# Kernel tuning notes

Measured on AMD Instinct MI355X. Metric: run time of the kernel, lower is better.

## Reference

```python
import jax, jax.numpy as jnp
import numpy as np

B, N = 8, 1000
EMB, K, F1E, F1V, MSG = 4, 3, 2, 3, 2


def cross_concat(h):
    # h: [b, n, d] -> [b, n, n, 2d], interleaving (h_i, h_j) per feature (stack axis=-1 then reshape)
    b, n, d = h.shape
    hi = jnp.broadcast_to(h[:, :, None, :], (b, n, n, d))
    hj = jnp.broadcast_to(h[:, None, :, :], (b, n, n, d))
    return jnp.stack((hi, hj), axis=-1).reshape(b, n, n, 2 * d)


def setup_inputs() -> dict:
    key = jax.random.key(0)
    ks = jax.random.split(key, 16)
    p = lambda k, s: (jax.random.normal(k, s, dtype=jnp.float32) * 0.1)
    return {
        "x": jax.random.normal(ks[0], (B, N), dtype=jnp.float32),
        "W1_emb": p(ks[1], (1, EMB)), "b1_emb": p(ks[2], (EMB,)),
        "W2_emb": p(ks[3], (1, EMB)), "b2_emb": p(ks[4], (EMB,)),
        "W_f1e": p(ks[5], (2 * EMB, F1E)), "b_f1e": p(ks[6], (F1E,)),
        "W_f2e": p(ks[7], (2 * F1V, K)), "b_f2e": p(ks[8], (K,)),
        "W_fk": p(ks[9], (K, 2 * EMB, MSG)), "b_fk": p(ks[10], (K, MSG)),
        "W_f1v": p(ks[11], (F1E, F1V)), "b_f1v": p(ks[12], (F1V,)),
        "W_f2v": p(ks[13], (MSG + 1, 1)), "b_f2v": p(ks[14], (1,)),
    }


def reference(x, W1_emb, b1_emb, W2_emb, b2_emb, W_f1e, b_f1e, W_f2e, b_f2e,
              W_fk, b_fk, W_f1v, b_f1v, W_f2v, b_f2v):
    x_ = x[..., None]                                  # [B,N,1]
    h1 = x_ @ W1_emb + b1_emb                          # [B,N,EMB]
    c = cross_concat(h1)                               # [B,N,N,2*EMB]
    h = jnp.sum(c @ W_f1e + b_f1e, axis=2)             # [B,N,F1E]
    h2 = h @ W_f1v + b_f1v                             # [B,N,F1V]
    c2 = cross_concat(h2)                              # [B,N,N,2*F1V]
    hsum = jnp.sum(c2, axis=0)                         # [N,N,2*F1V] (sum over batch)
    edge_logits = hsum @ W_f2e + b_f2e                 # [N,N,K]
    edge_probs = jax.nn.softmax(edge_logits, axis=-1)  # [N,N,K]
    h1_ = x_ @ W2_emb + b2_emb                         # [B,N,EMB]
    c3 = cross_concat(h1_)                             # [B,N,N,2*EMB]
    # K per-relation edge MLPs, stacked on the last axis -> [B,N,N,MSG,K]
    messages = jnp.einsum('bijd,kdm->bijmk', c3, W_fk) + b_fk.T
    # softmax-weighted combine, summed over receiver axis j and relation axis k
    v_e = jnp.einsum('ijk,bijmk->bim', edge_probs, messages)  # [B,N,MSG]
    h2_ = x_ + (jnp.concatenate((v_e, x_), axis=-1) @ W_f2v + b_f2v)
    return jnp.squeeze(h2_, axis=-1)                   # [B,N]
```

## Files before the change

kernel.cpp:

```cpp
#include <hip/hip_runtime.h>

#define NN 1000

__device__ __forceinline__ float wave_sum(float v) {
#pragma unroll
    for (int o = 32; o > 0; o >>= 1) v += __shfl_xor(v, o, 64);
    return v;
}

__global__ __launch_bounds__(256) void fused_kernel(
    const float* __restrict__ x,
    const float* __restrict__ W1, const float* __restrict__ b1,
    const float* __restrict__ W2, const float* __restrict__ b2,
    const float* __restrict__ Wf1e, const float* __restrict__ bf1e,
    const float* __restrict__ Wf2e, const float* __restrict__ bf2e,
    const float* __restrict__ Wfk, const float* __restrict__ bfk,
    const float* __restrict__ Wf1v, const float* __restrict__ bf1v,
    const float* __restrict__ Wf2v, const float* __restrict__ bf2v,
    float* __restrict__ out) {
    const int wave = threadIdx.x >> 6;
    const int lane = threadIdx.x & 63;
    const int i = blockIdx.x * 4 + wave;

    __shared__ float sA[4];

    float s = 0.f;
    const float4* x4 = reinterpret_cast<const float4*>(x);
    for (int q = threadIdx.x; q < 2 * NN; q += 256) {
        float4 v = x4[q];
        s += (v.x + v.y) + (v.z + v.w);
    }
    s = wave_sum(s);
    if (lane == 0) sA[wave] = s;

    float alpha[2];
#pragma unroll
    for (int f = 0; f < 2; ++f) {
        float a = 0.f;
#pragma unroll
        for (int e = 0; e < 4; ++e) a += W1[e] * Wf1e[(2 * e) * 2 + f];
        alpha[f] = (float)NN * a;
    }
    float gamma[3];
#pragma unroll
    for (int v = 0; v < 3; ++v) {
        float g = 0.f;
#pragma unroll
        for (int f = 0; f < 2; ++f) g += alpha[f] * Wf1v[f * 3 + v];
        gamma[v] = g;
    }
    float uA[6], cB[6], vA[6];
#pragma unroll
    for (int m = 0; m < 2; ++m)
#pragma unroll
        for (int k = 0; k < 3; ++k) {
            float ua = 0.f, ub = 0.f, va = 0.f, vb = 0.f;
#pragma unroll
            for (int e = 0; e < 4; ++e) {
                float wE = Wfk[k * 16 + (2 * e) * 2 + m];
                float wO = Wfk[k * 16 + (2 * e + 1) * 2 + m];
                ua += W2[e] * wE; ub += b2[e] * wE;
                va += W2[e] * wO; vb += b2[e] * wO;
            }
            uA[m * 3 + k] = ua;
            cB[m * 3 + k] = ub + vb + bfk[k * 2 + m];
            vA[m * 3 + k] = va;
        }

    __syncthreads();
    const float S = (sA[0] + sA[1]) + (sA[2] + sA[3]);

    float Bsum[2];
#pragma unroll
    for (int f = 0; f < 2; ++f) {
        float t0 = 0.f, t1 = 0.f;
#pragma unroll
        for (int e = 0; e < 4; ++e) {
            t0 += b1[e] * Wf1e[(2 * e) * 2 + f];
            t1 += (S * W1[e] + 8.f * (float)NN * b1[e]) * Wf1e[(2 * e + 1) * 2 + f];
        }
        Bsum[f] = 8.f * (float)NN * t0 + t1 + 8.f * (float)NN * bf1e[f];
    }
    float Ds[3];
#pragma unroll
    for (int v = 0; v < 3; ++v) {
        float d = 8.f * bf1v[v];
#pragma unroll
        for (int f = 0; f < 2; ++f) d += Bsum[f] * Wf1v[f * 3 + v];
        Ds[v] = d;
    }
    float PB[3], AiQ[3];
    {
        float xsi = 0.f;
#pragma unroll
        for (int b = 0; b < 8; ++b) xsi += x[b * NN + i];
#pragma unroll
        for (int k = 0; k < 3; ++k) {
            float PA = 0.f, QA = 0.f, pb = 0.f, qb = 0.f;
#pragma unroll
            for (int v = 0; v < 3; ++v) {
                PA += gamma[v] * Wf2e[(2 * v) * 3 + k];
                QA += Ds[v]    * Wf2e[(2 * v) * 3 + k];
                pb += gamma[v] * Wf2e[(2 * v + 1) * 3 + k];
                qb += Ds[v]    * Wf2e[(2 * v + 1) * 3 + k];
            }
            PB[k]  = pb;
            AiQ[k] = PA * xsi + QA + bf2e[k] + qb;
        }
    }

    const float ai0 = AiQ[0], ai1 = AiQ[1], ai2 = AiQ[2];
    const float pb0 = PB[0], pb1 = PB[1], pb2 = PB[2];
    float Q0 = 0.f, Q1 = 0.f, Q2 = 0.f;
    float R[8][3];
#pragma unroll
    for (int b = 0; b < 8; ++b)
#pragma unroll
        for (int k = 0; k < 3; ++k) R[b][k] = 0.f;

    for (int j4 = lane; j4 < NN / 4; j4 += 64) {
        float4 v[8];
#pragma unroll
        for (int b = 0; b < 8; ++b)
            v[b] = *reinterpret_cast<const float4*>(x + b * NN + 4 * j4);
        const float* vf = reinterpret_cast<const float*>(v);
#pragma unroll
        for (int u = 0; u < 4; ++u) {
            float xs = 0.f;
#pragma unroll
            for (int b = 0; b < 8; ++b) xs += vf[b * 4 + u];
            float l0 = ai0 + pb0 * xs, l1 = ai1 + pb1 * xs, l2 = ai2 + pb2 * xs;
            float mx = fmaxf(l0, fmaxf(l1, l2));
            float e0 = __expf(l0 - mx), e1 = __expf(l1 - mx), e2 = __expf(l2 - mx);
            float inv = 1.f / (e0 + e1 + e2);
            float p0 = e0 * inv, p1 = e1 * inv, p2 = e2 * inv;
            Q0 += p0; Q1 += p1; Q2 += p2;
#pragma unroll
            for (int b = 0; b < 8; ++b) {
                float xb = vf[b * 4 + u];
                R[b][0] += p0 * xb;
                R[b][1] += p1 * xb;
                R[b][2] += p2 * xb;
            }
        }
    }

    Q0 = wave_sum(Q0); Q1 = wave_sum(Q1); Q2 = wave_sum(Q2);
#pragma unroll
    for (int b = 0; b < 8; ++b) {
        R[b][0] = wave_sum(R[b][0]);
        R[b][1] = wave_sum(R[b][1]);
        R[b][2] = wave_sum(R[b][2]);
    }

    if (lane < 8) {
        const int b = lane;
        float xi = x[b * NN + i];
        float Rk0 = R[b][0], Rk1 = R[b][1], Rk2 = R[b][2];
        float ve[2];
#pragma unroll
        for (int m = 0; m < 2; ++m) {
            ve[m] = Q0 * (uA[m * 3 + 0] * xi + cB[m * 3 + 0]) + vA[m * 3 + 0] * Rk0
                  + Q1 * (uA[m * 3 + 1] * xi + cB[m * 3 + 1]) + vA[m * 3 + 1] * Rk1
                  + Q2 * (uA[m * 3 + 2] * xi + cB[m * 3 + 2]) + vA[m * 3 + 2] * Rk2;
        }
        out[b * NN + i] = xi + ve[0] * Wf2v[0] + ve[1] * Wf2v[1] + xi * Wf2v[2] + bf2v[0];
    }
}

extern "C" void kernel_launch(void* const* d_in, const int* in_sizes, int n_in,
                              void* d_out, int out_size, void* d_ws, size_t ws_size,
                              hipStream_t stream) {
    const float* x    = (const float*)d_in[0];
    const float* W1   = (const float*)d_in[1];
    const float* b1   = (const float*)d_in[2];
    const float* W2   = (const float*)d_in[3];
    const float* b2   = (const float*)d_in[4];
    const float* Wf1e = (const float*)d_in[5];
    const float* bf1e = (const float*)d_in[6];
    const float* Wf2e = (const float*)d_in[7];
    const float* bf2e = (const float*)d_in[8];
    const float* Wfk  = (const float*)d_in[9];
    const float* bfk  = (const float*)d_in[10];
    const float* Wf1v = (const float*)d_in[11];
    const float* bf1v = (const float*)d_in[12];
    const float* Wf2v = (const float*)d_in[13];
    const float* bf2v = (const float*)d_in[14];

    fused_kernel<<<NN / 4, 256, 0, stream>>>(x, W1, b1, W2, b2, Wf1e, bf1e,
                                             Wf2e, bf2e, Wfk, bfk, Wf1v, bf1v,
                                             Wf2v, bf2v, (float*)d_out);
}
```

Before: 97.51 us.

## Keep each wave's x tile in registers and drop the block barrier

Each wave now loads its entire 8x1000 slice of x into registers once, as a 4x8 float4 array. It computes the global sum S from those registers with a wave reduction instead of a block-cooperative pass followed by shared memory and __syncthreads. The main softmax/accumulate loop then reuses the register-held data rather than reloading x from global memory. This removes the second full read of x and the block barrier, at the cost of about 128 extra VGPRs per thread, which may reduce occupancy or cause spills.

Measured after the change: 93.94 us. 1.04x faster.

```diff
diff --git a/kernel.cpp b/kernel.cpp
--- a/kernel.cpp
+++ b/kernel.cpp
@@ -22,16 +22,27 @@
     const int lane = threadIdx.x & 63;
     const int i = blockIdx.x * 4 + wave;
 
-    __shared__ float sA[4];
+    float4 v[4][8];
+#pragma unroll
+    for (int t = 0; t < 4; ++t) {
+        const int j4 = lane + 64 * t;
+        if (j4 < NN / 4) {
+#pragma unroll
+            for (int b = 0; b < 8; ++b)
+                v[t][b] = *reinterpret_cast<const float4*>(x + b * NN + 4 * j4);
+        }
+    }
 
     float s = 0.f;
-    const float4* x4 = reinterpret_cast<const float4*>(x);
-    for (int q = threadIdx.x; q < 2 * NN; q += 256) {
-        float4 v = x4[q];
-        s += (v.x + v.y) + (v.z + v.w);
+#pragma unroll
+    for (int t = 0; t < 4; ++t) {
+        if (lane + 64 * t < NN / 4) {
+#pragma unroll
+            for (int b = 0; b < 8; ++b)
+                s += (v[t][b].x + v[t][b].y) + (v[t][b].z + v[t][b].w);
+        }
     }
-    s = wave_sum(s);
-    if (lane == 0) sA[wave] = s;
+    const float S = wave_sum(s);
 
     float alpha[2];
 #pragma unroll
@@ -43,13 +54,13 @@
     }
     float gamma[3];
 #pragma unroll
-    for (int v = 0; v < 3; ++v) {
+    for (int vv = 0; vv < 3; ++vv) {
         float g = 0.f;
 #pragma unroll
-        for (int f = 0; f < 2; ++f) g += alpha[f] * Wf1v[f * 3 + v];
-        gamma[v] = g;
+        for (int f = 0; f < 2; ++f) g += alpha[f] * Wf1v[f * 3 + vv];
+        gamma[vv] = g;
     }
-    float uA[6], cB[6], vA[6];
+    float uA[6], cB[6], vAc[6];
 #pragma unroll
     for (int m = 0; m < 2; ++m)
 #pragma unroll
@@ -62,14 +73,10 @@
                 ua += W2[e] * wE; ub += b2[e] * wE;
                 va += W2[e] * wO; vb += b2[e] * wO;
             }
-            uA[m * 3 + k] = ua;
-            cB[m * 3 + k] = ub + vb + bfk[k * 2 + m];
-            vA[m * 3 + k] = va;
+            uA[m * 3 + k]  = ua;
+            cB[m * 3 + k]  = ub + vb + bfk[k * 2 + m];
+            vAc[m * 3 + k] = va;
         }
-
-    __syncthreads();
-    const float S = (sA[0] + sA[1]) + (sA[2] + sA[3]);
-
     float Bsum[2];
 #pragma unroll
     for (int f = 0; f < 2; ++f) {
@@ -83,11 +90,11 @@
     }
     float Ds[3];
 #pragma unroll
-    for (int v = 0; v < 3; ++v) {
-        float d = 8.f * bf1v[v];
+    for (int vv = 0; vv < 3; ++vv) {
+        float d = 8.f * bf1v[vv];
 #pragma unroll
-        for (int f = 0; f < 2; ++f) d += Bsum[f] * Wf1v[f * 3 + v];
-        Ds[v] = d;
+        for (int f = 0; f < 2; ++f) d += Bsum[f] * Wf1v[f * 3 + vv];
+        Ds[vv] = d;
     }
     float PB[3], AiQ[3];
     {
@@ -98,11 +105,11 @@
         for (int k = 0; k < 3; ++k) {
             float PA = 0.f, QA = 0.f, pb = 0.f, qb = 0.f;
 #pragma unroll
-            for (int v = 0; v < 3; ++v) {
-                PA += gamma[v] * Wf2e[(2 * v) * 3 + k];
-                QA += Ds[v]    * Wf2e[(2 * v) * 3 + k];
-                pb += gamma[v] * Wf2e[(2 * v + 1) * 3 + k];
-                qb += Ds[v]    * Wf2e[(2 * v + 1) * 3 + k];
+            for (int vv = 0; vv < 3; ++vv) {
+                PA += gamma[vv] * Wf2e[(2 * vv) * 3 + k];
+                QA += Ds[vv]    * Wf2e[(2 * vv) * 3 + k];
+                pb += gamma[vv] * Wf2e[(2 * vv + 1) * 3 + k];
+                qb += Ds[vv]    * Wf2e[(2 * vv + 1) * 3 + k];
             }
             PB[k]  = pb;
             AiQ[k] = PA * xsi + QA + bf2e[k] + qb;
@@ -118,29 +125,28 @@
 #pragma unroll
         for (int k = 0; k < 3; ++k) R[b][k] = 0.f;
 
-    for (int j4 = lane; j4 < NN / 4; j4 += 64) {
-        float4 v[8];
 #pragma unroll
-        for (int b = 0; b < 8; ++b)
-            v[b] = *reinterpret_cast<const float4*>(x + b * NN + 4 * j4);
-        const float* vf = reinterpret_cast<const float*>(v);
+    for (int t = 0; t < 4; ++t) {
+        if (lane + 64 * t < NN / 4) {
+            const float* vf = reinterpret_cast<const float*>(v[t]);
 #pragma unroll
-        for (int u = 0; u < 4; ++u) {
-            float xs = 0.f;
+            for (int u = 0; u < 4; ++u) {
+                float xs = 0.f;
 #pragma unroll
-            for (int b = 0; b < 8; ++b) xs += vf[b * 4 + u];
-            float l0 = ai0 + pb0 * xs, l1 = ai1 + pb1 * xs, l2 = ai2 + pb2 * xs;
-            float mx = fmaxf(l0, fmaxf(l1, l2));
-            float e0 = __expf(l0 - mx), e1 = __expf(l1 - mx), e2 = __expf(l2 - mx);
-            float inv = 1.f / (e0 + e1 + e2);
-            float p0 = e0 * inv, p1 = e1 * inv, p2 = e2 * inv;
-            Q0 += p0; Q1 += p1; Q2 += p2;
+                for (int b = 0; b < 8; ++b) xs += vf[b * 4 + u];
+                float l0 = ai0 + pb0 * xs, l1 = ai1 + pb1 * xs, l2 = ai2 + pb2 * xs;
+                float mx = fmaxf(l0, fmaxf(l1, l2));
+                float e0 = __expf(l0 - mx), e1 = __expf(l1 - mx), e2 = __expf(l2 - mx);
+                float inv = 1.f / (e0 + e1 + e2);
+                float p0 = e0 * inv, p1 = e1 * inv, p2 = e2 * inv;
+                Q0 += p0; Q1 += p1; Q2 += p2;
 #pragma unroll
-            for (int b = 0; b < 8; ++b) {
-                float xb = vf[b * 4 + u];
-                R[b][0] += p0 * xb;
-                R[b][1] += p1 * xb;
-                R[b][2] += p2 * xb;
+                for (int b = 0; b < 8; ++b) {
+                    float xb = vf[b * 4 + u];
+                    R[b][0] += p0 * xb;
+                    R[b][1] += p1 * xb;
+                    R[b][2] += p2 * xb;
+                }
             }
         }
     }
@@ -160,9 +166,9 @@
         float ve[2];
 #pragma unroll
         for (int m = 0; m < 2; ++m) {
-            ve[m] = Q0 * (uA[m * 3 + 0] * xi + cB[m * 3 + 0]) + vA[m * 3 + 0] * Rk0
-                  + Q1 * (uA[m * 3 + 1] * xi + cB[m * 3 + 1]) + vA[m * 3 + 1] * Rk1
-                  + Q2 * (uA[m * 3 + 2] * xi + cB[m * 3 + 2]) + vA[m * 3 + 2] * Rk2;
+            ve[m] = Q0 * (uA[m * 3 + 0] * xi + cB[m * 3 + 0]) + vAc[m * 3 + 0] * Rk0
+                  + Q1 * (uA[m * 3 + 1] * xi + cB[m * 3 + 1]) + vAc[m * 3 + 1] * Rk1
+                  + Q2 * (uA[m * 3 + 2] * xi + cB[m * 3 + 2]) + vAc[m * 3 + 2] * Rk2;
         }
         out[b * NN + i] = xi + ve[0] * Wf2v[0] + ve[1] * Wf2v[1] + xi * Wf2v[2] + bf2v[0];
     }
```
